# Performance work log

Measured on AMD Instinct MI355X. Metric: run time of the kernel, lower is better.

Reference implementation:

```python
import jax, jax.numpy as jnp
from jax import lax
import numpy as np

N, I, O = 64, 8, 8
B = 512
S_EX, S_PHI, S_RHO = 10, 60, 60  # S_phi must equal S_rho (alpha loops feed S_rho-sized h into the GRUs)
N_ACTIONS, N_ROLES = 5, 7


def _gru(x, h, Wih, Whh, bih, bhh):
    # torch.nn.GRUCell math
    gi = x @ Wih.T + bih
    gh = h @ Whh.T + bhh
    ir, iz, inn = jnp.split(gi, 3, axis=-1)
    hr, hz, hn = jnp.split(gh, 3, axis=-1)
    r = jax.nn.sigmoid(ir + hr)
    zg = jax.nn.sigmoid(iz + hz)
    n = jnp.tanh(inn + r * hn)
    return (1.0 - zg) * n + zg * h


def setup_inputs() -> dict:
    key = jax.random.key(0)
    ks = jax.random.split(key, 24)
    f32 = jnp.float32
    z = jax.random.normal(ks[0], (B, N, S_EX), f32)
    dz = jax.random.normal(ks[1], (B, N, S_EX), f32)
    has = (jax.random.uniform(ks[2], (B, N)) < 0.9).astype(f32)
    adj = (jnp.triu(jax.random.uniform(ks[3], (N, N)), 1) > 0.7).astype(jnp.int32)

    def lin(k, o, i):
        return (jax.random.normal(k, (o, i), f32) * np.float32(1.0 / np.sqrt(i)))

    d = dict(z=z, dz=dz, has=has, adj=adj)
    d['Wih_f'] = lin(ks[4], 3 * S_PHI, S_RHO)
    d['Whh_f'] = lin(ks[5], 3 * S_PHI, S_PHI)
    d['bih_f'] = jax.random.normal(ks[6], (3 * S_PHI,), f32) * 0.02
    d['bhh_f'] = jax.random.normal(ks[7], (3 * S_PHI,), f32) * 0.02
    d['Wih_b'] = lin(ks[8], 3 * S_PHI, S_RHO)
    d['Whh_b'] = lin(ks[9], 3 * S_PHI, S_PHI)
    d['bih_b'] = jax.random.normal(ks[10], (3 * S_PHI,), f32) * 0.02
    d['bhh_b'] = jax.random.normal(ks[11], (3 * S_PHI,), f32) * 0.02
    d['Wf'] = lin(ks[12], S_RHO, S_PHI + 2 * S_EX)
    d['bf'] = jax.random.normal(ks[13], (S_RHO,), f32) * 0.02
    d['Wb'] = lin(ks[14], S_RHO, S_PHI + 2 * S_EX)
    d['bb'] = jax.random.normal(ks[15], (S_RHO,), f32) * 0.02
    d['Wa'] = lin(ks[16], N_ACTIONS, 2 * S_PHI)
    d['ba'] = jax.random.normal(ks[17], (N_ACTIONS,), f32) * 0.02
    d['Wc'] = lin(ks[18], 1, 2 * S_PHI)
    d['bc'] = jax.random.normal(ks[19], (1,), f32) * 0.02
    d['Wu'] = lin(ks[20], N_ROLES, 2 * S_RHO)
    d['bu'] = jax.random.normal(ks[21], (N_ROLES,), f32) * 0.02
    return d


def reference(z, dz, has, adj,
              Wih_f, Whh_f, bih_f, bhh_f,
              Wih_b, Whh_b, bih_b, bhh_b,
              Wf, bf, Wb, bb, Wa, ba, Wc, bc, Wu, bu):
    Bn, Nn = has.shape
    dt = z.dtype
    adjf = adj.astype(dt)

    # ---- forward sweep over nodes in ascending order ----
    def fwd_outer(rho, i):
        def inner(h, j):
            hn = _gru(rho[j], h, Wih_f, Whh_f, bih_f, bhh_f)
            blend = adjf[j, i] * has[:, j][:, None]  # edge exists AND source node present
            return h + blend * (hn - h), None
        h, _ = lax.scan(inner, jnp.zeros((Bn, S_PHI), dt), jnp.arange(Nn))
        rho_i = jnp.tanh(jnp.concatenate([h, z[:, i], dz[:, i]], 1) @ Wf.T + bf)
        return rho.at[i].set(rho_i), None

    rho_f, _ = lax.scan(fwd_outer, jnp.zeros((Nn, Bn, S_RHO), dt), jnp.arange(Nn))

    # ---- backward sweep over nodes in descending order ----
    def bwd_outer(rho, i):
        def inner(h, j):
            hn = _gru(rho[j], h, Wih_b, Whh_b, bih_b, bhh_b)
            blend = adjf[i, j] * has[:, j][:, None]  # out-edges of i, visited descending
            return h + blend * (hn - h), None
        h, _ = lax.scan(inner, jnp.zeros((Bn, S_PHI), dt), jnp.arange(Nn - 1, -1, -1))
        rho_i = jnp.concatenate([h, z[:, i], dz[:, i]], 1) @ Wb.T + bb
        return rho.at[i].set(rho_i), None

    rho_b, _ = lax.scan(bwd_outer, jnp.zeros((Nn, Bn, S_RHO), dt), jnp.arange(Nn - 1, -1, -1))

    # ---- aggregate outputs (last O nodes) and inputs (first I nodes) ----
    h = jnp.zeros((Bn, S_RHO), dt)
    for i in range(N - O, N):
        hn = _gru(rho_f[i], h, Wih_f, Whh_f, bih_f, bhh_f)
        h = h + has[:, i][:, None] * (hn - h)
    alpha_f = h
    h = jnp.zeros((Bn, S_RHO), dt)
    for i in reversed(range(I)):
        hn = _gru(rho_b[i], h, Wih_b, Whh_b, bih_b, bhh_b)
        h = h + has[:, i][:, None] * (hn - h)
    alpha_b = h

    ab = jnp.concatenate([alpha_f, alpha_b], 1)
    omega = ab @ Wa.T + ba          # [B, 5]
    value = ab @ Wc.T + bc          # [B, 1]

    feats = jnp.concatenate([rho_f, rho_b], -1)           # [N, B, 2*S_rho]
    psi = jnp.einsum('nbs,rs->brn', feats, Wu) + bu[None, :, None]  # [B, 7, N]
    m = has[:, None, :]
    psi = -60.0 * (1.0 - m) + psi * m  # interpolate(-60, psi, has)

    instr_prob = jax.nn.softmax(omega, axis=1)
    role_prob = jax.nn.softmax(psi, axis=2)
    return instr_prob, role_prob, value
```

## Files before the change

### kernel.cpp

```cpp
#include <hip/hip_runtime.h>
#include <hip/hip_bf16.h>

#define NN 64
#define BATCH 512
#define SP 60
#define SG 180
#define SEX 10
#define CATD 80
#define NA 5
#define NR 7
#define OO 8
#define II 8

typedef unsigned long long u64;
typedef unsigned short u16;
typedef unsigned int u32;
typedef unsigned char u8;

#define OFF_Z     0
#define OFF_DZ    327680
#define OFF_HAS   655360
#define OFF_WIHF  688128
#define OFF_WHHF  698928
#define OFF_BIHF  709728
#define OFF_BHHF  709908
#define OFF_WIHB  710088
#define OFF_WHHB  720888
#define OFF_BIHB  731688
#define OFF_BHHB  731868
#define OFF_WF    732048
#define OFF_BF    736848
#define OFF_WB    736908
#define OFF_BB    741708
#define OFF_WA    741768
#define OFF_BA    742368
#define OFF_WC    742373
#define OFF_BC    742493
#define OFF_WU    742494
#define OFF_BU    743334
#define CONV_TOTAL 743341
#define OFF_FLAG  743342
#define OFF_RHOF  743344
#define OFF_RHOB  (OFF_RHOF + 1966080)
#define OFF_ALF   (OFF_RHOB + 1966080)
#define OFF_ALB   (OFF_ALF + 30720)
#define OUT_TOTAL 232448

typedef _Float16 f16;
typedef _Float16 half2_t __attribute__((ext_vector_type(2)));
typedef _Float16 f16x8 __attribute__((ext_vector_type(8)));
typedef float f32x4 __attribute__((ext_vector_type(4)));

__device__ __forceinline__ float us2f(u16 v){
  return __uint_as_float(((u32)v) << 16);
}
__device__ __forceinline__ u16 f2bf(float f){
  __hip_bfloat16 h = __float2bfloat16(f);
  return *reinterpret_cast<u16*>(&h);
}
__device__ __forceinline__ float rcp_(float x){ return __builtin_amdgcn_rcpf(x); }
__device__ __forceinline__ float sigm(float x){
  return rcp_(1.f + __expf(-x));
}
__device__ __forceinline__ float tanh_(float x){
  float e = __expf(2.f*fabsf(x));
  float t = 1.f - 2.f*rcp_(e + 1.f);
  return copysignf(t, x);
}
__device__ __forceinline__ u32 pack2(float a, float b){
  half2_t h; h[0] = (f16)a; h[1] = (f16)b;
  return __builtin_bit_cast(u32, h);
}
__device__ __forceinline__ float fdot2_(u32 a, u32 b, float c){
  return __builtin_amdgcn_fdot2(__builtin_bit_cast(half2_t, a),
                                __builtin_bit_cast(half2_t, b), c, false);
}
__device__ __forceinline__ f16x8 bc16(uint4 v){ return __builtin_bit_cast(f16x8, v); }
__device__ __forceinline__ f32x4 mfma16(f16x8 a, f16x8 b, f32x4 c){
  return __builtin_amdgcn_mfma_f32_16x16x32_f16(a, b, c, 0, 0, 0);
}

struct HP { uint4 q[8]; };
__device__ __forceinline__ u32 hpc(const HP& p, int k){
  const uint4& v = p.q[k>>2];
  switch(k&3){ case 0: return v.x; case 1: return v.y; case 2: return v.z; default: return v.w; }
}

__device__ __forceinline__ int detect_bf16(const u32* w){
  int f = 0;
  for (int i=0;i<256;i++) f |= (w[i] == 0x3F803F80u) ? 1 : 0;
  return f;
}

__global__ __launch_bounds__(256) void conv_in(
  const void* z, const void* dz, const void* has,
  const void* WihF, const void* WhhF, const void* bihF, const void* bhhF,
  const void* WihB, const void* WhhB, const void* bihB, const void* bhhB,
  const void* Wf_, const void* bf_, const void* Wb_, const void* bb_,
  const void* Wa, const void* ba, const void* Wc, const void* bc,
  const void* Wu, const void* bu, float* ws)
{
  const int isbf = detect_bf16((const u32*)has);
  if (blockIdx.x == 0 && threadIdx.x == 0) ws[OFF_FLAG] = (float)isbf;
  int idx = blockIdx.x*256 + threadIdx.x;
  if (idx >= CONV_TOTAL) return;
  const void* src; int loc;
  if      (idx < OFF_DZ  ){ src=z;    loc=idx-OFF_Z;    }
  else if (idx < OFF_HAS ){ src=dz;   loc=idx-OFF_DZ;   }
  else if (idx < OFF_WIHF){ src=has;  loc=idx-OFF_HAS;  }
  else if (idx < OFF_WHHF){ src=WihF; loc=idx-OFF_WIHF; }
  else if (idx < OFF_BIHF){ src=WhhF; loc=idx-OFF_WHHF; }
  else if (idx < OFF_BHHF){ src=bihF; loc=idx-OFF_BIHF; }
  else if (idx < OFF_WIHB){ src=bhhF; loc=idx-OFF_BHHF; }
  else if (idx < OFF_WHHB){ src=WihB; loc=idx-OFF_WIHB; }
  else if (idx < OFF_BIHB){ src=WhhB; loc=idx-OFF_WHHB; }
  else if (idx < OFF_BHHB){ src=bihB; loc=idx-OFF_BIHB; }
  else if (idx < OFF_WF  ){ src=bhhB; loc=idx-OFF_BHHB; }
  else if (idx < OFF_BF  ){ src=Wf_;  loc=idx-OFF_WF;   }
  else if (idx < OFF_WB  ){ src=bf_;  loc=idx-OFF_BF;   }
  else if (idx < OFF_BB  ){ src=Wb_;  loc=idx-OFF_WB;   }
  else if (idx < OFF_WA  ){ src=bb_;  loc=idx-OFF_BB;   }
  else if (idx < OFF_BA  ){ src=Wa;   loc=idx-OFF_WA;   }
  else if (idx < OFF_WC  ){ src=ba;   loc=idx-OFF_BA;   }
  else if (idx < OFF_BC  ){ src=Wc;   loc=idx-OFF_WC;   }
  else if (idx < OFF_WU  ){ src=bc;   loc=idx-OFF_BC;   }
  else if (idx < OFF_BU  ){ src=Wu;   loc=idx-OFF_WU;   }
  else                    { src=bu;   loc=idx-OFF_BU;   }
  float v = isbf ? us2f(((const u16*)src)[loc]) : ((const float*)src)[loc];
  ws[idx] = v;
}

__global__ __launch_bounds__(64, 1) void dir_kernel(const int* __restrict__ adj,
                                                    float* __restrict__ ws)
{
  const int u   = threadIdx.x;
  const int ml  = u & 15;
  const int q   = u >> 4;
  const int bid = blockIdx.x;
  const int bwd = bid >> 9;
  const int b   = bid & 511;

  const float* Wih  = ws + (bwd ? OFF_WIHB : OFF_WIHF);
  const float* Whh  = ws + (bwd ? OFF_WHHB : OFF_WHHF);
  const float* bih  = ws + (bwd ? OFF_BIHB : OFF_BIHF);
  const float* bhh  = ws + (bwd ? OFF_BHHB : OFF_BHHF);
  const float* Wcat = ws + (bwd ? OFF_WB   : OFF_WF);
  const float* bcat = ws + (bwd ? OFF_BB   : OFF_BF);
  const float* zc   = ws + OFF_Z;
  const float* dzc  = ws + OFF_DZ;
  const float* hasc = ws + OFF_HAS;
  float* rho   = ws + (bwd ? OFF_RHOB : OFF_RHOF);
  float* alpha = ws + (bwd ? OFF_ALB  : OFF_ALF);

  __shared__ uint4 sH4[65][9];
  __shared__ uint4 sRhoPad[8];
  __shared__ uint4 sRhoHist[8][8];
  __shared__ float sRhoOut[NN][SP];
  __shared__ u32 sZp[NN][5];
  __shared__ u32 sDZp[NN][5];
  __shared__ float sHas[NN];
  __shared__ u64 sRowM[NN];
  __shared__ u8 sConsL[NN][64];
  __shared__ int sConsCnt[NN];

  #define ROWB(I) ((char*)&sH4[(I)][0])
  const u32 BIASW = 0x3C000000u;

  u64 rowm = 0;
  {
    for (int j=0;j<64;j++) rowm |= ((u64)(adj[u*64+j]!=0))<<j;
    sRowM[u] = rowm;
    sHas[u] = hasc[b*NN + u];
    for (int idx=u; idx<65*9; idx+=64){
      uint4 v = {0,0,0,0};
      if (idx % 9 == 7) v.w = BIASW;
      ((uint4*)sH4)[idx] = v;
    }
    if (u < 8){ uint4 v={0,0,0,0}; if (u==7) v.w = BIASW; sRhoPad[u]=v; }
    { uint4 v={0,0,0,0}; if ((u&7)==7) v.w = BIASW; ((uint4*)sRhoHist)[u]=v; }
    for (int idx=u; idx<NN*5; idx+=64){
      int n2=idx/5, p2=idx%5;
      sZp [n2][p2] = pack2(zc [(size_t)b*NN*SEX + n2*SEX + 2*p2],
                           zc [(size_t)b*NN*SEX + n2*SEX + 2*p2+1]);
      sDZp[n2][p2] = pack2(dzc[(size_t)b*NN*SEX + n2*SEX + 2*p2],
                           dzc[(size_t)b*NN*SEX + n2*SEX + 2*p2+1]);
    }
  }
  __syncthreads();
  {
    u64 cm = 0;
    if (bwd) for (int i2=0;i2<64;i2++) cm |= ((sRowM[i2]>>u)&1ULL)<<i2;
    u64 m = bwd ? cm : rowm;
    int c = 0;
    while (m){ int i2 = (int)__builtin_ctzll(m); m &= m-1; sConsL[u][c++] = (u8)i2; }
    sConsCnt[u] = c;
  }

  f16x8 Ar[4][4], Az[4][4], Anh[4][2], Ani[4][2];
  #pragma unroll
  for (int mt=0; mt<4; mt++){
    const int R = 16*mt + ml;
    const bool rok = (R < SP);
    #pragma unroll
    for (int kt=0; kt<4; kt++){
      f16x8 vr, vz;
      #pragma unroll
      for (int j=0;j<8;j++){
        const int K = 32*kt + 8*q + j;
        float wr=0.f, wz=0.f;
        if (rok){
          if (K < SP){ wr = Whh[R*SP+K]; wz = Whh[(60+R)*SP+K]; }
          else if (K >= 64 && K < 64+SP){ wr = Wih[R*SP+(K-64)]; wz = Wih[(60+R)*SP+(K-64)]; }
          else if (K == 127){ wr = bhh[R]+bih[R]; wz = bhh[60+R]+bih[60+R]; }
        }
        vr[j]=(f16)wr; vz[j]=(f16)wz;
      }
      Ar[mt][kt]=vr; Az[mt][kt]=vz;
    }
    #pragma unroll
    for (int kt=0; kt<2; kt++){
      f16x8 vn, vi;
      #pragma unroll
      for (int j=0;j<8;j++){
        const int K = 32*kt + 8*q + j;
        float wn=0.f, wi=0.f;
        if (rok){
          if (K < SP){ wn = Whh[(120+R)*SP+K]; wi = Wih[(120+R)*SP+K]; }
          else if (K == 63){ wn = bhh[120+R]; wi = bih[120+R]; }
        }
        vn[j]=(f16)wn; vi[j]=(f16)wi;
      }
      Anh[mt][kt]=vn; Ani[mt][kt]=vi;
    }
  }

  u32 wc[40];
  #pragma unroll
  for (int k=0;k<40;k++) wc[k] = pack2(Wcat[u*CATD + 2*k], Wcat[u*CATD + 2*k+1]);
  const float bct = bcat[u];
  __syncthreads();

  auto gatepass = [&](f16x8 Bh0, f16x8 Bh1, f16x8 Br0, f16x8 Br1,
                      const f32x4* Gn, int ci, bool wr, float bl){
    f32x4 Dr[4], Dz[4], Dn[4];
    #pragma unroll
    for (int mt=0;mt<4;mt++){
      f32x4 a={0,0,0,0};
      a = mfma16(Ar[mt][0], Bh0, a); a = mfma16(Ar[mt][1], Bh1, a);
      a = mfma16(Ar[mt][2], Br0, a); a = mfma16(Ar[mt][3], Br1, a);
      Dr[mt] = a;
      f32x4 c2={0,0,0,0};
      c2 = mfma16(Az[mt][0], Bh0, c2); c2 = mfma16(Az[mt][1], Bh1, c2);
      c2 = mfma16(Az[mt][2], Br0, c2); c2 = mfma16(Az[mt][3], Br1, c2);
      Dz[mt] = c2;
      f32x4 d={0,0,0,0};
      d = mfma16(Anh[mt][0], Bh0, d); d = mfma16(Anh[mt][1], Bh1, d);
      Dn[mt] = d;
    }
    #pragma unroll
    for (int mt=0;mt<4;mt++){
      char* rp = ROWB(ci) + 32*mt + 8*q;
      uint2 h2 = *(uint2*)rp;
      half2_t ha = __builtin_bit_cast(half2_t, h2.x);
      half2_t hb = __builtin_bit_cast(half2_t, h2.y);
      float hold[4] = { (float)ha[0], (float)ha[1], (float)hb[0], (float)hb[1] };
      float hw[4];
      #pragma unroll
      for (int reg=0;reg<4;reg++){
        float r_ = sigm(Dr[mt][reg]);
        float zg = sigm(Dz[mt][reg]);
        float nv = tanh_(Gn[mt][reg] + r_*Dn[mt][reg]);
        float hn_ = (1.f - zg)*nv + zg*hold[reg];
        hw[reg] = (bl != 0.f) ? hn_ : hold[reg];
      }
      if (wr && !(mt==3 && q==3)){
        uint2 o; o.x = pack2(hw[0],hw[1]); o.y = pack2(hw[2],hw[3]);
        *(uint2*)rp = o;
      }
    }
  };

  int t = bwd ? 63 : 0;
  const int dt = bwd ? -1 : 1;
  for (int s=0; s<64; s++, t+=dt){
    {
      HP ht;
      { const uint4* _r=(const uint4*)&sH4[t][0];
        #pragma unroll
        for (int _k=0;_k<8;_k++) ht.q[_k]=_r[_k]; }
      float c0 = bct, c1 = 0.f, c2 = 0.f, c3 = 0.f;
      #pragma unroll
      for (int k=0;k<28;k+=4){
        c0 = fdot2_(wc[k],   hpc(ht,k),   c0);
        c1 = fdot2_(wc[k+1], hpc(ht,k+1), c1);
        c2 = fdot2_(wc[k+2], hpc(ht,k+2), c2);
        c3 = fdot2_(wc[k+3], hpc(ht,k+3), c3);
      }
      c0 = fdot2_(wc[28], hpc(ht,28), c0);
      c1 = fdot2_(wc[29], hpc(ht,29), c1);
      #pragma unroll
      for (int p2=0;p2<5;p2++){
        c2 = fdot2_(wc[30+p2], sZp [t][p2], c2);
        c3 = fdot2_(wc[35+p2], sDZp[t][p2], c3);
      }
      float acc = (c0 + c1) + (c2 + c3);
      float rv = bwd ? acc : tanh_(acc);
      if (u < SP){
        sRhoOut[t][u] = rv;
        *(f16*)((char*)&sRhoPad[0] + 2*u) = (f16)rv;
      }
      const int slot = bwd ? t : (t - (NN-OO));
      if (slot >= 0 && slot < 8 && u < SP)
        *(f16*)((char*)&sRhoHist[slot][0] + 2*u) = (f16)rv;
    }
    __syncthreads();

    const float blendT = sHas[t];
    const int cnt = sConsCnt[t];
    if (blendT != 0.f && cnt > 0){
      const f16x8 Br0 = bc16(sRhoPad[q]);
      const f16x8 Br1 = bc16(sRhoPad[4+q]);
      f32x4 Gn[4];
      #pragma unroll
      for (int mt=0;mt<4;mt++){
        f32x4 g={0,0,0,0};
        g = mfma16(Ani[mt][0], Br0, g);
        g = mfma16(Ani[mt][1], Br1, g);
        Gn[mt] = g;
      }
      for (int p=0; 16*p < cnt; p++){
        const int idxp = 16*p + ml;
        const int ci = (idxp < cnt) ? (int)sConsL[t][idxp] : 64;
        const f16x8 Bh0 = bc16(sH4[ci][q]);
        const f16x8 Bh1 = bc16(sH4[ci][4+q]);
        gatepass(Bh0, Bh1, Br0, Br1, Gn, ci, idxp < cnt, 1.0f);
      }
    }
    __syncthreads();
  }

  for (int idx=u; idx<NN*SP; idx+=64){
    int n2 = idx/SP, s2 = idx%SP;
    rho[((size_t)n2*BATCH + b)*SP + s2] = sRhoOut[n2][s2];
  }

  for (int s2=0; s2<8; s2++){
    const int i = bwd ? (7 - s2) : (NN - OO + s2);
    const int slot = bwd ? i : (i - (NN-OO));
    const f16x8 Th0 = bc16(sH4[64][q]);
    const f16x8 Th1 = bc16(sH4[64][4+q]);
    const f16x8 Tr0 = bc16(sRhoHist[slot][q]);
    const f16x8 Tr1 = bc16(sRhoHist[slot][4+q]);
    f32x4 Gt[4];
    #pragma unroll
    for (int mt=0;mt<4;mt++){
      f32x4 g={0,0,0,0};
      g = mfma16(Ani[mt][0], Tr0, g);
      g = mfma16(Ani[mt][1], Tr1, g);
      Gt[mt] = g;
    }
    gatepass(Th0, Th1, Tr0, Tr1, Gt, 64, ml==0, sHas[i]);
    __syncthreads();
  }
  if (u < SP) alpha[(size_t)b*SP + u] = (float)*(const f16*)(ROWB(64) + 2*u);
  #undef ROWB
}

__global__ __launch_bounds__(256, 1) void head_kernel(float* __restrict__ ws,
                                                      void* __restrict__ outp)
{
  const int b = blockIdx.x;
  const int tid = threadIdx.x;
  const int isbf = (ws[OFF_FLAG] != 0.f);
  const float* hasc   = ws + OFF_HAS;
  const float* WaC    = ws + OFF_WA;
  const float* baC    = ws + OFF_BA;
  const float* WcC    = ws + OFF_WC;
  const float* bcC    = ws + OFF_BC;
  const float* WuC    = ws + OFF_WU;
  const float* buC    = ws + OFF_BU;
  const float* rhoF   = ws + OFF_RHOF;
  const float* rhoB   = ws + OFF_RHOB;
  const float* alphaF = ws + OFF_ALF;
  const float* alphaB = ws + OFF_ALB;

  __shared__ float sF[NN][121];
  __shared__ float sAB[120];
  __shared__ float sWu[NR*120];
  __shared__ float sHasR[NN];
  __shared__ float sPsi[NR][NN];
  __shared__ float sRed[NR][2];
  __shared__ float sOm[NA];

  auto wout = [&](int idx, float v){
    if (isbf) ((u16*)outp)[idx] = f2bf(v);
    else      ((float*)outp)[idx] = v;
  };

  for (int idx=tid; idx<NN*SP; idx+=256){
    int n = idx/SP, s = idx%SP;
    sF[n][s]    = rhoF[((size_t)n*BATCH + b)*SP + s];
    sF[n][60+s] = rhoB[((size_t)n*BATCH + b)*SP + s];
  }
  for (int idx=tid; idx<120; idx+=256)
    sAB[idx] = (idx<60) ? alphaF[(size_t)b*SP + idx] : alphaB[(size_t)b*SP + idx-60];
  for (int idx=tid; idx<NR*120; idx+=256) sWu[idx] = WuC[idx];
  for (int idx=tid; idx<NN; idx+=256) sHasR[idx] = hasc[b*NN + idx];
  __syncthreads();

  for (int idx=tid; idx<NR*NN; idx+=256){
    int r = idx/NN, n = idx%NN;
    float acc = buC[r];
    for (int s=0;s<120;s++) acc += sF[n][s]*sWu[r*120+s];
    sPsi[r][n] = (sHasR[n] != 0.f) ? acc : -60.f;
  }
  if (tid >= 64 && tid < 64+NA){
    int a = tid - 64;
    float acc = baC[a];
    for (int s=0;s<120;s++) acc += sAB[s]*WaC[a*120+s];
    sOm[a] = acc;
  }
  if (tid == 70){
    float acc = bcC[0];
    for (int s=0;s<120;s++) acc += sAB[s]*WcC[s];
    wout(2560 + BATCH*NR*NN + b, acc);
  }
  __syncthreads();

  if (tid < NR){
    float m = -1e30f;
    for (int n=0;n<NN;n++) m = fmaxf(m, sPsi[tid][n]);
    float ssum = 0.f;
    for (int n=0;n<NN;n++) ssum += __expf(sPsi[tid][n]-m);
    sRed[tid][0] = m; sRed[tid][1] = 1.f/ssum;
  }
  if (tid == 8){
    float m = -1e30f;
    for (int a=0;a<NA;a++) m = fmaxf(m, sOm[a]);
    float e[NA]; float ssum = 0.f;
    for (int a=0;a<NA;a++){ e[a] = __expf(sOm[a]-m); ssum += e[a]; }
    for (int a=0;a<NA;a++) wout(b*NA + a, e[a]/ssum);
  }
  __syncthreads();

  for (int idx=tid; idx<NR*NN; idx+=256){
    int r = idx/NN, n = idx%NN;
    float v = __expf(sPsi[r][n]-sRed[r][0]) * sRed[r][1];
    wout(2560 + (size_t)b*NR*NN + idx, v);
  }
}

extern "C" void kernel_launch(void* const* d_in, const int* in_sizes, int n_in,
                              void* d_out, int out_size, void* d_ws, size_t ws_size,
                              hipStream_t stream)
{
  const int* adj = (const int*)d_in[3];
  float* ws = (float*)d_ws;

  conv_in<<<(CONV_TOTAL+255)/256, 256, 0, stream>>>(
      d_in[0], d_in[1], d_in[2],
      d_in[4], d_in[5], d_in[6], d_in[7],
      d_in[8], d_in[9], d_in[10], d_in[11],
      d_in[12], d_in[13], d_in[14], d_in[15],
      d_in[16], d_in[17], d_in[18], d_in[19],
      d_in[20], d_in[21], ws);

  dir_kernel<<<1024, 64, 0, stream>>>(adj, ws);

  head_kernel<<<512, 256, 0, stream>>>(ws, d_out);
}
```

Measured before the change: 302.0 us.

## Fold input conversion into dir and head kernels; parallelize head reductions

Removes the separate conv_in kernel that copied every input into a float workspace. dir_kernel and head_kernel now read the raw inputs directly, each running its own bf16/fp32 detection and converting per element. This saves one launch and a full pass over z/dz/has through global memory. The head kernel's omega/value dot products and softmax max/sum reductions are spread over 32-lane groups with shuffles instead of single threads, at the cost of repeating the format detection in every block.

Result: no change. 305.0 us (+1.0%).

```diff
diff --git a/kernel.cpp b/kernel.cpp
--- a/kernel.cpp
+++ b/kernel.cpp
@@ -17,33 +17,10 @@
 typedef unsigned int u32;
 typedef unsigned char u8;
 
-#define OFF_Z     0
-#define OFF_DZ    327680
-#define OFF_HAS   655360
-#define OFF_WIHF  688128
-#define OFF_WHHF  698928
-#define OFF_BIHF  709728
-#define OFF_BHHF  709908
-#define OFF_WIHB  710088
-#define OFF_WHHB  720888
-#define OFF_BIHB  731688
-#define OFF_BHHB  731868
-#define OFF_WF    732048
-#define OFF_BF    736848
-#define OFF_WB    736908
-#define OFF_BB    741708
-#define OFF_WA    741768
-#define OFF_BA    742368
-#define OFF_WC    742373
-#define OFF_BC    742493
-#define OFF_WU    742494
-#define OFF_BU    743334
-#define CONV_TOTAL 743341
-#define OFF_FLAG  743342
-#define OFF_RHOF  743344
-#define OFF_RHOB  (OFF_RHOF + 1966080)
-#define OFF_ALF   (OFF_RHOB + 1966080)
-#define OFF_ALB   (OFF_ALF + 30720)
+#define OFF_RHOF  0
+#define OFF_RHOB  1966080
+#define OFF_ALF   3932160
+#define OFF_ALB   3962880
 #define OUT_TOTAL 232448
 
 typedef _Float16 f16;
@@ -92,46 +69,17 @@
   return f;
 }
 
-__global__ __launch_bounds__(256) void conv_in(
-  const void* z, const void* dz, const void* has,
-  const void* WihF, const void* WhhF, const void* bihF, const void* bhhF,
-  const void* WihB, const void* WhhB, const void* bihB, const void* bhhB,
-  const void* Wf_, const void* bf_, const void* Wb_, const void* bb_,
-  const void* Wa, const void* ba, const void* Wc, const void* bc,
-  const void* Wu, const void* bu, float* ws)
-{
-  const int isbf = detect_bf16((const u32*)has);
-  if (blockIdx.x == 0 && threadIdx.x == 0) ws[OFF_FLAG] = (float)isbf;
-  int idx = blockIdx.x*256 + threadIdx.x;
-  if (idx >= CONV_TOTAL) return;
-  const void* src; int loc;
-  if      (idx < OFF_DZ  ){ src=z;    loc=idx-OFF_Z;    }
-  else if (idx < OFF_HAS ){ src=dz;   loc=idx-OFF_DZ;   }
-  else if (idx < OFF_WIHF){ src=has;  loc=idx-OFF_HAS;  }
-  else if (idx < OFF_WHHF){ src=WihF; loc=idx-OFF_WIHF; }
-  else if (idx < OFF_BIHF){ src=WhhF; loc=idx-OFF_WHHF; }
-  else if (idx < OFF_BHHF){ src=bihF; loc=idx-OFF_BIHF; }
-  else if (idx < OFF_WIHB){ src=bhhF; loc=idx-OFF_BHHF; }
-  else if (idx < OFF_WHHB){ src=WihB; loc=idx-OFF_WIHB; }
-  else if (idx < OFF_BIHB){ src=WhhB; loc=idx-OFF_WHHB; }
-  else if (idx < OFF_BHHB){ src=bihB; loc=idx-OFF_BIHB; }
-  else if (idx < OFF_WF  ){ src=bhhB; loc=idx-OFF_BHHB; }
-  else if (idx < OFF_BF  ){ src=Wf_;  loc=idx-OFF_WF;   }
-  else if (idx < OFF_WB  ){ src=bf_;  loc=idx-OFF_BF;   }
-  else if (idx < OFF_BB  ){ src=Wb_;  loc=idx-OFF_WB;   }
-  else if (idx < OFF_WA  ){ src=bb_;  loc=idx-OFF_BB;   }
-  else if (idx < OFF_BA  ){ src=Wa;   loc=idx-OFF_WA;   }
-  else if (idx < OFF_WC  ){ src=ba;   loc=idx-OFF_BA;   }
-  else if (idx < OFF_BC  ){ src=Wc;   loc=idx-OFF_WC;   }
-  else if (idx < OFF_WU  ){ src=bc;   loc=idx-OFF_BC;   }
-  else if (idx < OFF_BU  ){ src=Wu;   loc=idx-OFF_WU;   }
-  else                    { src=bu;   loc=idx-OFF_BU;   }
-  float v = isbf ? us2f(((const u16*)src)[loc]) : ((const float*)src)[loc];
-  ws[idx] = v;
-}
-
-__global__ __launch_bounds__(64, 1) void dir_kernel(const int* __restrict__ adj,
-                                                    float* __restrict__ ws)
+__global__ __launch_bounds__(64, 1) void dir_kernel(
+  const int* __restrict__ adj,
+  const void* __restrict__ zv, const void* __restrict__ dzv,
+  const void* __restrict__ hasv,
+  const void* __restrict__ WihFv, const void* __restrict__ WhhFv,
+  const void* __restrict__ bihFv, const void* __restrict__ bhhFv,
+  const void* __restrict__ WihBv, const void* __restrict__ WhhBv,
+  const void* __restrict__ bihBv, const void* __restrict__ bhhBv,
+  const void* __restrict__ WfV, const void* __restrict__ bfV,
+  const void* __restrict__ WbV, const void* __restrict__ bbV,
+  float* __restrict__ ws)
 {
   const int u   = threadIdx.x;
   const int ml  = u & 15;
@@ -140,15 +88,17 @@
   const int bwd = bid >> 9;
   const int b   = bid & 511;
 
-  const float* Wih  = ws + (bwd ? OFF_WIHB : OFF_WIHF);
-  const float* Whh  = ws + (bwd ? OFF_WHHB : OFF_WHHF);
-  const float* bih  = ws + (bwd ? OFF_BIHB : OFF_BIHF);
-  const float* bhh  = ws + (bwd ? OFF_BHHB : OFF_BHHF);
-  const float* Wcat = ws + (bwd ? OFF_WB   : OFF_WF);
-  const float* bcat = ws + (bwd ? OFF_BB   : OFF_BF);
-  const float* zc   = ws + OFF_Z;
-  const float* dzc  = ws + OFF_DZ;
-  const float* hasc = ws + OFF_HAS;
+  const int isbf = detect_bf16((const u32*)hasv);
+  auto gf = [&](const void* p, int i)->float{
+    return isbf ? us2f(((const u16*)p)[i]) : ((const float*)p)[i];
+  };
+
+  const void* Wihv  = bwd ? WihBv : WihFv;
+  const void* Whhv  = bwd ? WhhBv : WhhFv;
+  const void* bihv  = bwd ? bihBv : bihFv;
+  const void* bhhv  = bwd ? bhhBv : bhhFv;
+  const void* Wcatv = bwd ? WbV   : WfV;
+  const void* bcatv = bwd ? bbV   : bfV;
   float* rho   = ws + (bwd ? OFF_RHOB : OFF_RHOF);
   float* alpha = ws + (bwd ? OFF_ALB  : OFF_ALF);
 
@@ -170,7 +120,7 @@
   {
     for (int j=0;j<64;j++) rowm |= ((u64)(adj[u*64+j]!=0))<<j;
     sRowM[u] = rowm;
-    sHas[u] = hasc[b*NN + u];
+    sHas[u] = gf(hasv, b*NN + u);
     for (int idx=u; idx<65*9; idx+=64){
       uint4 v = {0,0,0,0};
       if (idx % 9 == 7) v.w = BIASW;
@@ -180,10 +130,10 @@
     { uint4 v={0,0,0,0}; if ((u&7)==7) v.w = BIASW; ((uint4*)sRhoHist)[u]=v; }
     for (int idx=u; idx<NN*5; idx+=64){
       int n2=idx/5, p2=idx%5;
-      sZp [n2][p2] = pack2(zc [(size_t)b*NN*SEX + n2*SEX + 2*p2],
-                           zc [(size_t)b*NN*SEX + n2*SEX + 2*p2+1]);
-      sDZp[n2][p2] = pack2(dzc[(size_t)b*NN*SEX + n2*SEX + 2*p2],
-                           dzc[(size_t)b*NN*SEX + n2*SEX + 2*p2+1]);
+      sZp [n2][p2] = pack2(gf(zv,  (size_t)b*NN*SEX + n2*SEX + 2*p2),
+                           gf(zv,  (size_t)b*NN*SEX + n2*SEX + 2*p2+1));
+      sDZp[n2][p2] = pack2(gf(dzv, (size_t)b*NN*SEX + n2*SEX + 2*p2),
+                           gf(dzv, (size_t)b*NN*SEX + n2*SEX + 2*p2+1));
     }
   }
   __syncthreads();
@@ -209,9 +159,9 @@
         const int K = 32*kt + 8*q + j;
         float wr=0.f, wz=0.f;
         if (rok){
-          if (K < SP){ wr = Whh[R*SP+K]; wz = Whh[(60+R)*SP+K]; }
-          else if (K >= 64 && K < 64+SP){ wr = Wih[R*SP+(K-64)]; wz = Wih[(60+R)*SP+(K-64)]; }
-          else if (K == 127){ wr = bhh[R]+bih[R]; wz = bhh[60+R]+bih[60+R]; }
+          if (K < SP){ wr = gf(Whhv, R*SP+K); wz = gf(Whhv, (60+R)*SP+K); }
+          else if (K >= 64 && K < 64+SP){ wr = gf(Wihv, R*SP+(K-64)); wz = gf(Wihv, (60+R)*SP+(K-64)); }
+          else if (K == 127){ wr = gf(bhhv,R)+gf(bihv,R); wz = gf(bhhv,60+R)+gf(bihv,60+R); }
         }
         vr[j]=(f16)wr; vz[j]=(f16)wz;
       }
@@ -225,8 +175,8 @@
         const int K = 32*kt + 8*q + j;
         float wn=0.f, wi=0.f;
         if (rok){
-          if (K < SP){ wn = Whh[(120+R)*SP+K]; wi = Wih[(120+R)*SP+K]; }
-          else if (K == 63){ wn = bhh[120+R]; wi = bih[120+R]; }
+          if (K < SP){ wn = gf(Whhv,(120+R)*SP+K); wi = gf(Wihv,(120+R)*SP+K); }
+          else if (K == 63){ wn = gf(bhhv,120+R); wi = gf(bihv,120+R); }
         }
         vn[j]=(f16)wn; vi[j]=(f16)wi;
       }
@@ -236,8 +186,9 @@
 
   u32 wc[40];
   #pragma unroll
-  for (int k=0;k<40;k++) wc[k] = pack2(Wcat[u*CATD + 2*k], Wcat[u*CATD + 2*k+1]);
-  const float bct = bcat[u];
+  for (int k=0;k<40;k++)
+    wc[k] = pack2(gf(Wcatv, u*CATD + 2*k), gf(Wcatv, u*CATD + 2*k+1));
+  const float bct = gf(bcatv, u);
   __syncthreads();
 
   auto gatepass = [&](f16x8 Bh0, f16x8 Bh1, f16x8 Br0, f16x8 Br1,
@@ -366,19 +317,19 @@
   #undef ROWB
 }
 
-__global__ __launch_bounds__(256, 1) void head_kernel(float* __restrict__ ws,
-                                                      void* __restrict__ outp)
+__global__ __launch_bounds__(256, 1) void head_kernel(
+  const void* __restrict__ hasv,
+  const void* __restrict__ Wav, const void* __restrict__ bav,
+  const void* __restrict__ Wcv, const void* __restrict__ bcv,
+  const void* __restrict__ Wuv, const void* __restrict__ buv,
+  const float* __restrict__ ws, void* __restrict__ outp)
 {
   const int b = blockIdx.x;
   const int tid = threadIdx.x;
-  const int isbf = (ws[OFF_FLAG] != 0.f);
-  const float* hasc   = ws + OFF_HAS;
-  const float* WaC    = ws + OFF_WA;
-  const float* baC    = ws + OFF_BA;
-  const float* WcC    = ws + OFF_WC;
-  const float* bcC    = ws + OFF_BC;
-  const float* WuC    = ws + OFF_WU;
-  const float* buC    = ws + OFF_BU;
+  const int isbf = detect_bf16((const u32*)hasv);
+  auto gf = [&](const void* p, int i)->float{
+    return isbf ? us2f(((const u16*)p)[i]) : ((const float*)p)[i];
+  };
   const float* rhoF   = ws + OFF_RHOF;
   const float* rhoB   = ws + OFF_RHOB;
   const float* alphaF = ws + OFF_ALF;
@@ -404,42 +355,47 @@
   }
   for (int idx=tid; idx<120; idx+=256)
     sAB[idx] = (idx<60) ? alphaF[(size_t)b*SP + idx] : alphaB[(size_t)b*SP + idx-60];
-  for (int idx=tid; idx<NR*120; idx+=256) sWu[idx] = WuC[idx];
-  for (int idx=tid; idx<NN; idx+=256) sHasR[idx] = hasc[b*NN + idx];
+  for (int idx=tid; idx<NR*120; idx+=256) sWu[idx] = gf(Wuv, idx);
+  for (int idx=tid; idx<NN; idx+=256) sHasR[idx] = gf(hasv, b*NN + idx);
   __syncthreads();
 
   for (int idx=tid; idx<NR*NN; idx+=256){
     int r = idx/NN, n = idx%NN;
-    float acc = buC[r];
+    float acc = gf(buv, r);
     for (int s=0;s<120;s++) acc += sF[n][s]*sWu[r*120+s];
     sPsi[r][n] = (sHasR[n] != 0.f) ? acc : -60.f;
   }
-  if (tid >= 64 && tid < 64+NA){
-    int a = tid - 64;
-    float acc = baC[a];
-    for (int s=0;s<120;s++) acc += sAB[s]*WaC[a*120+s];
-    sOm[a] = acc;
-  }
-  if (tid == 70){
-    float acc = bcC[0];
-    for (int s=0;s<120;s++) acc += sAB[s]*WcC[s];
-    wout(2560 + BATCH*NR*NN + b, acc);
+  if (tid < 192){
+    int r = tid >> 5, j = tid & 31;
+    float acc = 0.f;
+    if (r < NA){
+      for (int s=j; s<120; s+=32) acc += sAB[s]*gf(Wav, r*120+s);
+    } else {
+      for (int s=j; s<120; s+=32) acc += sAB[s]*gf(Wcv, s);
+    }
+    for (int off=16; off; off>>=1) acc += __shfl_xor(acc, off, 32);
+    if (j == 0){
+      if (r < NA) sOm[r] = acc + gf(bav, r);
+      else wout(2560 + BATCH*NR*NN + b, acc + gf(bcv, 0));
+    }
   }
   __syncthreads();
 
-  if (tid < NR){
-    float m = -1e30f;
-    for (int n=0;n<NN;n++) m = fmaxf(m, sPsi[tid][n]);
-    float ssum = 0.f;
-    for (int n=0;n<NN;n++) ssum += __expf(sPsi[tid][n]-m);
-    sRed[tid][0] = m; sRed[tid][1] = 1.f/ssum;
-  }
-  if (tid == 8){
+  if (tid < 224){
+    int r = tid >> 5, j = tid & 31;
+    float a = sPsi[r][j], c = sPsi[r][j+32];
+    float m = fmaxf(a, c);
+    for (int off=16; off; off>>=1) m = fmaxf(m, __shfl_xor(m, off, 32));
+    float e = __expf(a-m) + __expf(c-m);
+    for (int off=16; off; off>>=1) e += __shfl_xor(e, off, 32);
+    if (j == 0){ sRed[r][0] = m; sRed[r][1] = 1.f/e; }
+  } else if (tid == 224){
     float m = -1e30f;
     for (int a=0;a<NA;a++) m = fmaxf(m, sOm[a]);
     float e[NA]; float ssum = 0.f;
     for (int a=0;a<NA;a++){ e[a] = __expf(sOm[a]-m); ssum += e[a]; }
-    for (int a=0;a<NA;a++) wout(b*NA + a, e[a]/ssum);
+    float inv = 1.f/ssum;
+    for (int a=0;a<NA;a++) wout(b*NA + a, e[a]*inv);
   }
   __syncthreads();
 
@@ -457,15 +413,14 @@
   const int* adj = (const int*)d_in[3];
   float* ws = (float*)d_ws;
 
-  conv_in<<<(CONV_TOTAL+255)/256, 256, 0, stream>>>(
+  dir_kernel<<<1024, 64, 0, stream>>>(adj,
       d_in[0], d_in[1], d_in[2],
       d_in[4], d_in[5], d_in[6], d_in[7],
       d_in[8], d_in[9], d_in[10], d_in[11],
       d_in[12], d_in[13], d_in[14], d_in[15],
-      d_in[16], d_in[17], d_in[18], d_in[19],
-      d_in[20], d_in[21], ws);
-
-  dir_kernel<<<1024, 64, 0, stream>>>(adj, ws);
-
-  head_kernel<<<512, 256, 0, stream>>>(ws, d_out);
-}
+      ws);
+
+  head_kernel<<<512, 256, 0, stream>>>(
+      d_in[2], d_in[16], d_in[17], d_in[18], d_in[19],
+      d_in[20], d_in[21], ws, d_out);
+}
```
